# Performance work log

Measured on AMD Instinct MI355X. Metric: run time of the kernel, lower is better.

## Reference

```python
import jax, jax.numpy as jnp
import numpy as np


def setup_inputs() -> dict:
    key = jax.random.key(0)
    k1, k2 = jax.random.split(key)
    a_bar = jax.random.normal(k1, (32, 512, 512), dtype=jnp.float32)
    b_bar = jax.random.normal(k2, (32, 512, 512), dtype=jnp.float32)
    return {"a_bar": a_bar, "b_bar": b_bar}


def reference(a_bar, b_bar):
    # e[b,i,j] = <a_bar[b,i,:], b_bar[b,j,:]>
    e = jnp.einsum("bid,bjd->bij", a_bar, b_bar)
    # a_tilde: row softmax (over j) then weighted sum of b rows
    attn_a = jax.nn.softmax(e, axis=2)            # [B, Sa, Sb]
    a_tilde = jnp.einsum("bij,bjd->bid", attn_a, b_bar)
    # b_tilde: column softmax (over i), transposed, times a_bar
    attn_b = jax.nn.softmax(e, axis=1)            # [B, Sa, Sb]
    b_tilde = jnp.einsum("bij,bid->bjd", attn_b, a_bar)
    m_a = jnp.concatenate([a_bar, a_tilde, a_bar - a_tilde, a_bar * a_tilde], axis=-1)
    m_b = jnp.concatenate([b_bar, b_tilde, b_bar - b_tilde, b_bar * b_tilde], axis=-1)
    return (m_a, m_b)
```

## Files before the change

kernel.cpp:

```cpp
#include <hip/hip_runtime.h>
#include <hip/hip_bf16.h>
#include <math.h>

#define B_   32
#define S_   512
#define SxS  (S_ * S_)
#define LOG2E 1.4426950408889634f

using frag_ab = __attribute__((ext_vector_type(8))) short;
using frag_cd = __attribute__((ext_vector_type(4))) float;

__device__ inline short f2bf(float x) {
    __hip_bfloat16 h = __float2bfloat16(x);
    return *reinterpret_cast<short*>(&h);
}
__device__ inline float bf2f(short s) {
    __hip_bfloat16 h = *reinterpret_cast<__hip_bfloat16*>(&s);
    return __bfloat162float(h);
}
__device__ __forceinline__ int swz(int r) { return (r ^ (r >> 3)) & 7; }

__device__ __forceinline__ void async16(const short* g, short* l) {
    __builtin_amdgcn_global_load_lds(
        (const __attribute__((address_space(1))) void*)g,
        (__attribute__((address_space(3))) void*)l,
        16, 0, 0);
}

__global__ __launch_bounds__(256) void k_prep(const float* __restrict__ A,
                                              const float* __restrict__ Bm,
                                              short* __restrict__ PA,
                                              short* __restrict__ PB,
                                              short* __restrict__ Va,
                                              short* __restrict__ Vb)
{
    const int z   = blockIdx.z;
    const int b   = z & 31;
    const int isB = z >> 5;
    const float* X = (isB ? Bm : A) + (size_t)b * SxS;
    short* P  = (isB ? PB : PA) + (size_t)b * (S_ * 1024);
    short* Vp = (isB ? Vb : Va) + (size_t)b * SxS;
    const float scale = isB ? 1.0f : LOG2E;

    const int i0 = blockIdx.y * 64, d0 = blockIdx.x * 64;

    __shared__ short T[64][72];

    const int sl = threadIdx.x & 7;
    const int il = threadIdx.x >> 3;

    #pragma unroll
    for (int p = 0; p < 2; ++p) {
        const int i    = il + 32 * p;
        const int rowg = i0 + i;
        const float* src = X + (size_t)rowg * S_ + d0 + sl * 8;
        const float4 v0 = *(const float4*)(src);
        const float4 v1 = *(const float4*)(src + 4);

        T[sl * 8 + 0][i] = f2bf(v0.x); T[sl * 8 + 1][i] = f2bf(v0.y);
        T[sl * 8 + 2][i] = f2bf(v0.z); T[sl * 8 + 3][i] = f2bf(v0.w);
        T[sl * 8 + 4][i] = f2bf(v1.x); T[sl * 8 + 5][i] = f2bf(v1.y);
        T[sl * 8 + 6][i] = f2bf(v1.z); T[sl * 8 + 7][i] = f2bf(v1.w);

        const float xs[8] = {v0.x, v0.y, v0.z, v0.w, v1.x, v1.y, v1.z, v1.w};
        frag_ab hi, lo;
        #pragma unroll
        for (int j = 0; j < 8; ++j) {
            const float x = xs[j] * scale;
            const short h = f2bf(x);
            hi[j] = h;
            lo[j] = f2bf(x - bf2f(h));
        }
        const int W = (d0 >> 5) + (sl >> 2);
        const int q = sl & 3;
        short* base = P + (size_t)rowg * 1024 + W * 64;
        *(frag_ab*)(base + (((2 * q)     ^ (rowg & 7)) * 8)) = hi;
        *(frag_ab*)(base + (((2 * q + 1) ^ (rowg & 7)) * 8)) = lo;
    }
    __syncthreads();

    const int pc = threadIdx.x & 7, dl = threadIdx.x >> 3;
    #pragma unroll
    for (int p = 0; p < 2; ++p) {
        const int d  = dl + 32 * p;
        const int dg = d0 + d;
        frag_ab t = *(const frag_ab*)&T[d][pc * 8];
        *(frag_ab*)(Vp + (size_t)dg * 512 + i0 + ((pc ^ (dg & 7)) * 8)) = t;
    }
}

__global__ __launch_bounds__(256) void k_gemm_e(const short* __restrict__ PA,
                                                const short* __restrict__ PB,
                                                float* __restrict__ E)
{
    const int lin     = blockIdx.x + (blockIdx.y << 2) + (blockIdx.z << 4);
    const int logical = ((lin & 7) << 6) + (lin >> 3);
    const int b  = logical >> 4;
    const int i0 = ((logical >> 2) & 3) * 128;
    const int j0 = (logical & 3) * 128;

    const short* Ab = PA + (size_t)b * (S_ * 1024);
    const short* Bb = PB + (size_t)b * (S_ * 1024);
    float* Eb = E + (size_t)b * SxS;

    __shared__ __align__(16) short As[128][64];
    __shared__ __align__(16) short Bs[128][64];

    const int tid  = threadIdx.x;
    const int wave = tid >> 6, lane = tid & 63;
    const int wr   = wave >> 1, wc = wave & 1;
    const int q    = lane >> 4, m = lane & 15;
    const int srow = lane >> 3, schunk = lane & 7;

    frag_cd zero = {0.f, 0.f, 0.f, 0.f};
    frag_cd acc[4][4];
    #pragma unroll
    for (int i = 0; i < 4; ++i)
        #pragma unroll
        for (int j = 0; j < 4; ++j) acc[i][j] = zero;

    for (int k0 = 0; k0 < S_; k0 += 32) {
        const int W = k0 >> 5;
        __syncthreads();
        #pragma unroll
        for (int p = 0; p < 4; ++p) {
            const int seg    = wave * 4 + p;
            const int rowg_a = i0 + seg * 8 + srow;
            const int rowg_b = j0 + seg * 8 + srow;
            async16(Ab + (size_t)rowg_a * 1024 + W * 64 + schunk * 8, &As[seg * 8][0]);
            async16(Bb + (size_t)rowg_b * 1024 + W * 64 + schunk * 8, &Bs[seg * 8][0]);
        }
        __syncthreads();

        frag_ab ah[4], al[4], bh[4], bl[4];
        #pragma unroll
        for (int t = 0; t < 4; ++t) {
            const int ra = wr * 64 + t * 16 + m;
            const int rb = wc * 64 + t * 16 + m;
            ah[t] = *(const frag_ab*)&As[ra][((2 * q)     ^ (ra & 7)) * 8];
            al[t] = *(const frag_ab*)&As[ra][((2 * q + 1) ^ (ra & 7)) * 8];
            bh[t] = *(const frag_ab*)&Bs[rb][((2 * q)     ^ (rb & 7)) * 8];
            bl[t] = *(const frag_ab*)&Bs[rb][((2 * q + 1) ^ (rb & 7)) * 8];
        }
        #pragma unroll
        for (int mt = 0; mt < 4; ++mt)
            #pragma unroll
            for (int nt = 0; nt < 4; ++nt) {
                acc[mt][nt] = __builtin_amdgcn_mfma_f32_16x16x32_bf16(ah[mt], bh[nt], acc[mt][nt], 0, 0, 0);
                acc[mt][nt] = __builtin_amdgcn_mfma_f32_16x16x32_bf16(ah[mt], bl[nt], acc[mt][nt], 0, 0, 0);
                acc[mt][nt] = __builtin_amdgcn_mfma_f32_16x16x32_bf16(al[mt], bh[nt], acc[mt][nt], 0, 0, 0);
            }
    }

    #pragma unroll
    for (int mt = 0; mt < 4; ++mt)
        #pragma unroll
        for (int nt = 0; nt < 4; ++nt) {
            const int rb  = i0 + wr * 64 + mt * 16 + q * 4;
            const int col = j0 + wc * 64 + nt * 16 + m;
            Eb[(size_t)(rb + 0) * S_ + col] = acc[mt][nt][0];
            Eb[(size_t)(rb + 1) * S_ + col] = acc[mt][nt][1];
            Eb[(size_t)(rb + 2) * S_ + col] = acc[mt][nt][2];
            Eb[(size_t)(rb + 3) * S_ + col] = acc[mt][nt][3];
        }
}

__global__ __launch_bounds__(512) void k_pv_fused(const float* __restrict__ E,
                                                  const short* __restrict__ Va,
                                                  const short* __restrict__ Vb,
                                                  const float* __restrict__ A,
                                                  const float* __restrict__ Bm,
                                                  float* __restrict__ Ma,
                                                  float* __restrict__ Mb)
{
    const int lin     = blockIdx.x;
    const int logical = ((lin & 7) << 6) + (lin >> 3);
    const int side = logical >> 8;
    const int b    = (logical >> 3) & 31;
    const int s0   = (logical & 7) * 64;

    const float* Eb  = E + (size_t)b * SxS;
    const short* Vg  = (side ? Va : Vb) + (size_t)b * SxS;
    const float* Xb  = (side ? Bm : A) + (size_t)b * SxS;
    float* Ob = (side ? Mb : Ma) + (size_t)b * S_ * 2048;

    __shared__ __align__(16) short Pl[64][512];
    __shared__ __align__(16) short Vs[512][64];
    __shared__ float riS[64];
    __shared__ float mS[64];

    float* scr  = (float*)&Vs[0][0];
    float* scr2 = scr + 4096;

    const int tid = threadIdx.x;

    if (side == 0) {
        const int r = tid >> 3, sub = tid & 7;
        const float* er = Eb + (size_t)(s0 + r) * S_;

        float mx = -INFINITY;
        #pragma unroll
        for (int fi = 0; fi < 8; ++fi) {
            const float* p = er + sub * 8 + fi * 64;
            const float4 u  = *(const float4*)p;
            const float4 u2 = *(const float4*)(p + 4);
            mx = fmaxf(mx, fmaxf(fmaxf(u.x, u.y), fmaxf(u.z, u.w)));
            mx = fmaxf(mx, fmaxf(fmaxf(u2.x, u2.y), fmaxf(u2.z, u2.w)));
        }
        mx = fmaxf(mx, __shfl_xor(mx, 1));
        mx = fmaxf(mx, __shfl_xor(mx, 2));
        mx = fmaxf(mx, __shfl_xor(mx, 4));

        float s = 0.f;
        const int sl = (sub ^ swz(r)) * 8;
        #pragma unroll
        for (int fi = 0; fi < 8; ++fi) {
            const float* p = er + sub * 8 + fi * 64;
            const float4 u  = *(const float4*)p;
            const float4 u2 = *(const float4*)(p + 4);
            const float xs[8] = {u.x, u.y, u.z, u.w, u2.x, u2.y, u2.z, u2.w};
            frag_ab pb;
            #pragma unroll
            for (int j = 0; j < 8; ++j) {
                const float pv = exp2f(xs[j] - mx);
                s += pv;
                pb[j] = f2bf(pv);
            }
            *(frag_ab*)&Pl[r][fi * 64 + sl] = pb;
        }
        s += __shfl_xor(s, 1);
        s += __shfl_xor(s, 2);
        s += __shfl_xor(s, 4);
        if (sub == 0) riS[r] = 1.0f / s;
    } else {
        const int ib = tid >> 3, sub = tid & 7;

        float pm[8];
        #pragma unroll
        for (int c = 0; c < 8; ++c) pm[c] = -INFINITY;
        #pragma unroll
        for (int ii = 0; ii < 8; ++ii) {
            const float* p = Eb + (size_t)(ib * 8 + ii) * S_ + s0 + sub * 8;
            const float4 u  = *(const float4*)p;
            const float4 u2 = *(const float4*)(p + 4);
            pm[0] = fmaxf(pm[0], u.x);  pm[1] = fmaxf(pm[1], u.y);
            pm[2] = fmaxf(pm[2], u.z);  pm[3] = fmaxf(pm[3], u.w);
            pm[4] = fmaxf(pm[4], u2.x); pm[5] = fmaxf(pm[5], u2.y);
            pm[6] = fmaxf(pm[6], u2.z); pm[7] = fmaxf(pm[7], u2.w);
        }
        #pragma unroll
        for (int c = 0; c < 8; ++c) scr[ib * 64 + sub * 8 + c] = pm[c];
        __syncthreads();
        {
            const int col = tid & 63, h = tid >> 6;
            float v = scr[(h * 8) * 64 + col];
            #pragma unroll
            for (int k = 1; k < 8; ++k) v = fmaxf(v, scr[(h * 8 + k) * 64 + col]);
            scr2[h * 64 + col] = v;
        }
        __syncthreads();
        if (tid < 64) {
            float v = scr2[tid];
            #pragma unroll
            for (int h = 1; h < 8; ++h) v = fmaxf(v, scr2[h * 64 + tid]);
            mS[tid] = v;
        }
        __syncthreads();

        float ps[8];
        frag_ab pb[8];
        #pragma unroll
        for (int c = 0; c < 8; ++c) ps[c] = 0.f;
        #pragma unroll
        for (int ii = 0; ii < 8; ++ii) {
            const float* p = Eb + (size_t)(ib * 8 + ii) * S_ + s0 + sub * 8;
            const float4 u  = *(const float4*)p;
            const float4 u2 = *(const float4*)(p + 4);
            const float xs[8] = {u.x, u.y, u.z, u.w, u2.x, u2.y, u2.z, u2.w};
            #pragma unroll
            for (int c = 0; c < 8; ++c) {
                const float pv = exp2f(xs[c] - mS[sub * 8 + c]);
                ps[c] += pv;
                pb[c][ii] = f2bf(pv);
            }
        }
        #pragma unroll
        for (int c = 0; c < 8; ++c) {
            const int cl = sub * 8 + c;
            *(frag_ab*)&Pl[cl][(ib >> 3) * 64 + (((ib & 7) ^ swz(cl)) * 8)] = pb[c];
        }
        __syncthreads();
        #pragma unroll
        for (int c = 0; c < 8; ++c) scr[ib * 64 + sub * 8 + c] = ps[c];
        __syncthreads();
        {
            const int col = tid & 63, h = tid >> 6;
            float v = 0.f;
            #pragma unroll
            for (int k = 0; k < 8; ++k) v += scr[(h * 8 + k) * 64 + col];
            scr2[h * 64 + col] = v;
        }
        __syncthreads();
        if (tid < 64) {
            float v = 0.f;
            #pragma unroll
            for (int h = 0; h < 8; ++h) v += scr2[h * 64 + tid];
            riS[tid] = 1.0f / v;
        }
    }

    const int wv = tid >> 6, lane = tid & 63;
    const int q = lane >> 4, m = lane & 15;

    frag_cd zero = {0.f, 0.f, 0.f, 0.f};
    frag_cd acc[4][4];
    #pragma unroll
    for (int i = 0; i < 4; ++i)
        #pragma unroll
        for (int j = 0; j < 4; ++j) acc[i][j] = zero;

    for (int k0 = 0; k0 < S_; k0 += 64) {
        __syncthreads();
        #pragma unroll
        for (int p = 0; p < 8; ++p) {
            const int d = p * 64 + wv * 8 + (lane >> 3);
            async16(Vg + (size_t)d * 512 + k0 + (lane & 7) * 8,
                    &Vs[p * 64 + wv * 8][0]);
        }
        __syncthreads();

        #pragma unroll
        for (int kk = 0; kk < 2; ++kk) {
            frag_ab af[4], bf[4];
            #pragma unroll
            for (int t = 0; t < 4; ++t) {
                const int row = t * 16 + m;
                af[t] = *(const frag_ab*)&Pl[row][k0 + (((kk * 4 + q) ^ swz(row)) * 8)];
                const int dl = wv * 64 + t * 16 + m;
                bf[t] = *(const frag_ab*)&Vs[dl][(((kk * 4 + q) ^ (dl & 7)) * 8)];
            }
            #pragma unroll
            for (int mt = 0; mt < 4; ++mt)
                #pragma unroll
                for (int nt = 0; nt < 4; ++nt)
                    acc[mt][nt] = __builtin_amdgcn_mfma_f32_16x16x32_bf16(af[mt], bf[nt], acc[mt][nt], 0, 0, 0);
        }
    }

    #pragma unroll
    for (int mt = 0; mt < 4; ++mt)
        #pragma unroll
        for (int nt = 0; nt < 4; ++nt) {
            const int col = wv * 64 + nt * 16 + m;
            #pragma unroll
            for (int rr = 0; rr < 4; ++rr) {
                const int rl   = mt * 16 + q * 4 + rr;
                const int rowg = s0 + rl;
                const float at = acc[mt][nt][rr] * riS[rl];
                const float xv = Xb[(size_t)rowg * S_ + col];
                float* o = Ob + (size_t)rowg * 2048 + col;
                o[0]    = xv;
                o[512]  = at;
                o[1024] = xv - at;
                o[1536] = xv * at;
            }
        }
}

extern "C" void kernel_launch(void* const* d_in, const int* in_sizes, int n_in,
                              void* d_out, int out_size, void* d_ws, size_t ws_size,
                              hipStream_t stream)
{
    const float* A  = (const float*)d_in[0];
    const float* Bm = (const float*)d_in[1];
    float* Ma = (float*)d_out;
    float* Mb = Ma + (size_t)B_ * S_ * 2048;

    float* E  = (float*)d_ws;
    short* Va = (short*)(E + (size_t)B_ * SxS);
    short* Vb = Va + (size_t)B_ * SxS;

    short* PA = (short*)d_out;
    short* PB = PA + (size_t)B_ * S_ * 1024;

    k_prep    <<<dim3(8, 8, 64), 256, 0, stream>>>(A, Bm, PA, PB, Va, Vb);
    k_gemm_e  <<<dim3(4, 4, 32), 256, 0, stream>>>(PA, PB, E);
    k_pv_fused<<<dim3(512),      512, 0, stream>>>(E, Va, Vb, A, Bm, Ma, Mb);
}
```

Before: 468.1 us.

## Split softmax statistics into separate kernels and shrink PV tiles for more blocks

Row and column softmax max and inverse-sum are now computed by two dedicated kernels and written to workspace. The PV kernel only reads these statistics and exponentiates. It now uses 32-row by 256-column tiles with 256 threads, giving 2048 blocks instead of 512 with a smaller LDS footprint. This aims to remove the serialized in-block reductions and barriers and to improve occupancy and load balance. The cost is more passes over the E matrix (two extra stat kernels, and each PV tile re-reads E for both d-halves) plus two extra launches.

```diff
diff --git a/kernel.cpp b/kernel.cpp
--- a/kernel.cpp
+++ b/kernel.cpp
@@ -165,54 +165,138 @@
         }
 }
 
-__global__ __launch_bounds__(512) void k_pv_fused(const float* __restrict__ E,
-                                                  const short* __restrict__ Va,
-                                                  const short* __restrict__ Vb,
-                                                  const float* __restrict__ A,
-                                                  const float* __restrict__ Bm,
-                                                  float* __restrict__ Ma,
-                                                  float* __restrict__ Mb)
-{
-    const int lin     = blockIdx.x;
-    const int logical = ((lin & 7) << 6) + (lin >> 3);
-    const int side = logical >> 8;
-    const int b    = (logical >> 3) & 31;
-    const int s0   = (logical & 7) * 64;
+__global__ __launch_bounds__(256) void k_rstats(const float* __restrict__ E,
+                                                float* __restrict__ rmax,
+                                                float* __restrict__ rinv)
+{
+    const int row  = blockIdx.x * 4 + (threadIdx.x >> 6);
+    const int lane = threadIdx.x & 63;
+    const float* er = E + (size_t)row * S_;
+
+    float4 v0 = *(const float4*)(er + lane * 4);
+    float4 v1 = *(const float4*)(er + 256 + lane * 4);
+
+    float m = fmaxf(fmaxf(fmaxf(v0.x, v0.y), fmaxf(v0.z, v0.w)),
+                    fmaxf(fmaxf(v1.x, v1.y), fmaxf(v1.z, v1.w)));
+    #pragma unroll
+    for (int off = 32; off >= 1; off >>= 1)
+        m = fmaxf(m, __shfl_xor(m, off));
+
+    float s = exp2f(v0.x - m) + exp2f(v0.y - m)
+            + exp2f(v0.z - m) + exp2f(v0.w - m)
+            + exp2f(v1.x - m) + exp2f(v1.y - m)
+            + exp2f(v1.z - m) + exp2f(v1.w - m);
+    #pragma unroll
+    for (int off = 32; off >= 1; off >>= 1)
+        s += __shfl_xor(s, off);
+
+    if (lane == 0) { rmax[row] = m; rinv[row] = 1.0f / s; }
+}
+
+__global__ __launch_bounds__(256) void k_cstats(const float* __restrict__ E,
+                                                float* __restrict__ cmax,
+                                                float* __restrict__ cinv)
+{
+    const int b  = blockIdx.x >> 3;
+    const int s0 = (blockIdx.x & 7) * 64;
+    const float* Eb = E + (size_t)b * SxS;
+
+    __shared__ float scr[32][64];
+    __shared__ float mS[64];
+
+    const int tid = threadIdx.x;
+    const int ib  = tid >> 3;
+    const int sub = tid & 7;
+
+    float pm[8];
+    #pragma unroll
+    for (int c = 0; c < 8; ++c) pm[c] = -INFINITY;
+    for (int ii = 0; ii < 16; ++ii) {
+        const float* p = Eb + (size_t)(ib * 16 + ii) * S_ + s0 + sub * 8;
+        const float4 u  = *(const float4*)p;
+        const float4 u2 = *(const float4*)(p + 4);
+        pm[0] = fmaxf(pm[0], u.x);  pm[1] = fmaxf(pm[1], u.y);
+        pm[2] = fmaxf(pm[2], u.z);  pm[3] = fmaxf(pm[3], u.w);
+        pm[4] = fmaxf(pm[4], u2.x); pm[5] = fmaxf(pm[5], u2.y);
+        pm[6] = fmaxf(pm[6], u2.z); pm[7] = fmaxf(pm[7], u2.w);
+    }
+    #pragma unroll
+    for (int c = 0; c < 8; ++c) scr[ib][sub * 8 + c] = pm[c];
+    __syncthreads();
+    if (tid < 64) {
+        float v = scr[0][tid];
+        #pragma unroll
+        for (int k = 1; k < 32; ++k) v = fmaxf(v, scr[k][tid]);
+        mS[tid] = v;
+        cmax[b * S_ + s0 + tid] = v;
+    }
+    __syncthreads();
+
+    float ps[8];
+    #pragma unroll
+    for (int c = 0; c < 8; ++c) ps[c] = 0.f;
+    for (int ii = 0; ii < 16; ++ii) {
+        const float* p = Eb + (size_t)(ib * 16 + ii) * S_ + s0 + sub * 8;
+        const float4 u  = *(const float4*)p;
+        const float4 u2 = *(const float4*)(p + 4);
+        const float xs[8] = {u.x, u.y, u.z, u.w, u2.x, u2.y, u2.z, u2.w};
+        #pragma unroll
+        for (int c = 0; c < 8; ++c) ps[c] += exp2f(xs[c] - mS[sub * 8 + c]);
+    }
+    __syncthreads();
+    #pragma unroll
+    for (int c = 0; c < 8; ++c) scr[ib][sub * 8 + c] = ps[c];
+    __syncthreads();
+    if (tid < 64) {
+        float v = 0.f;
+        #pragma unroll
+        for (int k = 0; k < 32; ++k) v += scr[k][tid];
+        cinv[b * S_ + s0 + tid] = 1.0f / v;
+    }
+}
+
+__global__ __launch_bounds__(256) void k_pv(const float* __restrict__ E,
+                                            const float* __restrict__ rmx_,
+                                            const float* __restrict__ rin_,
+                                            const float* __restrict__ cmx_,
+                                            const float* __restrict__ cin_,
+                                            const short* __restrict__ Va,
+                                            const short* __restrict__ Vb,
+                                            const float* __restrict__ A,
+                                            const float* __restrict__ Bm,
+                                            float* __restrict__ Ma,
+                                            float* __restrict__ Mb)
+{
+    const int lin = blockIdx.x;
+    const int wg  = ((lin & 7) << 8) | (lin >> 3);
+    const int side = wg >> 10;
+    const int b    = (wg >> 5) & 31;
+    const int rs   = (wg >> 1) & 15;
+    const int dh   = wg & 1;
+    const int s0   = rs * 32;
 
     const float* Eb  = E + (size_t)b * SxS;
+    const float* pmx = (side ? cmx_ : rmx_) + b * S_;
+    const float* piv = (side ? cin_ : rin_) + b * S_;
     const short* Vg  = (side ? Va : Vb) + (size_t)b * SxS;
     const float* Xb  = (side ? Bm : A) + (size_t)b * SxS;
     float* Ob = (side ? Mb : Ma) + (size_t)b * S_ * 2048;
 
-    __shared__ __align__(16) short Pl[64][512];
-    __shared__ __align__(16) short Vs[512][64];
-    __shared__ float riS[64];
-    __shared__ float mS[64];
-
-    float* scr  = (float*)&Vs[0][0];
-    float* scr2 = scr + 4096;
+    __shared__ __align__(16) short Pl[32][512];
+    __shared__ __align__(16) short Vs[256][64];
+    __shared__ float riS[32];
 
     const int tid = threadIdx.x;
+    const int wv  = tid >> 6, lane = tid & 63;
+    const int q   = lane >> 4, m = lane & 15;
+
+    if (tid < 32) riS[tid] = piv[s0 + tid];
 
     if (side == 0) {
-        const int r = tid >> 3, sub = tid & 7;
-        const float* er = Eb + (size_t)(s0 + r) * S_;
-
-        float mx = -INFINITY;
-        #pragma unroll
-        for (int fi = 0; fi < 8; ++fi) {
-            const float* p = er + sub * 8 + fi * 64;
-            const float4 u  = *(const float4*)p;
-            const float4 u2 = *(const float4*)(p + 4);
-            mx = fmaxf(mx, fmaxf(fmaxf(u.x, u.y), fmaxf(u.z, u.w)));
-            mx = fmaxf(mx, fmaxf(fmaxf(u2.x, u2.y), fmaxf(u2.z, u2.w)));
-        }
-        mx = fmaxf(mx, __shfl_xor(mx, 1));
-        mx = fmaxf(mx, __shfl_xor(mx, 2));
-        mx = fmaxf(mx, __shfl_xor(mx, 4));
-
-        float s = 0.f;
-        const int sl = (sub ^ swz(r)) * 8;
+        const int rl = tid >> 3, sub = tid & 7;
+        const float mx = pmx[s0 + rl];
+        const float* er = Eb + (size_t)(s0 + rl) * S_;
+        const int sl = (sub ^ swz(rl)) * 8;
         #pragma unroll
         for (int fi = 0; fi < 8; ++fi) {
             const float* p = er + sub * 8 + fi * 64;
@@ -221,101 +305,37 @@
             const float xs[8] = {u.x, u.y, u.z, u.w, u2.x, u2.y, u2.z, u2.w};
             frag_ab pb;
             #pragma unroll
-            for (int j = 0; j < 8; ++j) {
-                const float pv = exp2f(xs[j] - mx);
-                s += pv;
-                pb[j] = f2bf(pv);
-            }
-            *(frag_ab*)&Pl[r][fi * 64 + sl] = pb;
-        }
-        s += __shfl_xor(s, 1);
-        s += __shfl_xor(s, 2);
-        s += __shfl_xor(s, 4);
-        if (sub == 0) riS[r] = 1.0f / s;
+            for (int j = 0; j < 8; ++j) pb[j] = f2bf(exp2f(xs[j] - mx));
+            *(frag_ab*)&Pl[rl][fi * 64 + sl] = pb;
+        }
     } else {
-        const int ib = tid >> 3, sub = tid & 7;
-
-        float pm[8];
-        #pragma unroll
-        for (int c = 0; c < 8; ++c) pm[c] = -INFINITY;
+        const int ib = tid >> 2, cs = tid & 3;
+        float mloc[8];
+        #pragma unroll
+        for (int c = 0; c < 8; ++c) mloc[c] = pmx[s0 + cs * 8 + c];
+        frag_ab pb[8];
         #pragma unroll
         for (int ii = 0; ii < 8; ++ii) {
-            const float* p = Eb + (size_t)(ib * 8 + ii) * S_ + s0 + sub * 8;
-            const float4 u  = *(const float4*)p;
-            const float4 u2 = *(const float4*)(p + 4);
-            pm[0] = fmaxf(pm[0], u.x);  pm[1] = fmaxf(pm[1], u.y);
-            pm[2] = fmaxf(pm[2], u.z);  pm[3] = fmaxf(pm[3], u.w);
-            pm[4] = fmaxf(pm[4], u2.x); pm[5] = fmaxf(pm[5], u2.y);
-            pm[6] = fmaxf(pm[6], u2.z); pm[7] = fmaxf(pm[7], u2.w);
-        }
-        #pragma unroll
-        for (int c = 0; c < 8; ++c) scr[ib * 64 + sub * 8 + c] = pm[c];
-        __syncthreads();
-        {
-            const int col = tid & 63, h = tid >> 6;
-            float v = scr[(h * 8) * 64 + col];
-            #pragma unroll
-            for (int k = 1; k < 8; ++k) v = fmaxf(v, scr[(h * 8 + k) * 64 + col]);
-            scr2[h * 64 + col] = v;
-        }
-        __syncthreads();
-        if (tid < 64) {
-            float v = scr2[tid];
-            #pragma unroll
-            for (int h = 1; h < 8; ++h) v = fmaxf(v, scr2[h * 64 + tid]);
-            mS[tid] = v;
-        }
-        __syncthreads();
-
-        float ps[8];
-        frag_ab pb[8];
-        #pragma unroll
-        for (int c = 0; c < 8; ++c) ps[c] = 0.f;
-        #pragma unroll
-        for (int ii = 0; ii < 8; ++ii) {
-            const float* p = Eb + (size_t)(ib * 8 + ii) * S_ + s0 + sub * 8;
+            const float* p = Eb + (size_t)(ib * 8 + ii) * S_ + s0 + cs * 8;
             const float4 u  = *(const float4*)p;
             const float4 u2 = *(const float4*)(p + 4);
             const float xs[8] = {u.x, u.y, u.z, u.w, u2.x, u2.y, u2.z, u2.w};
             #pragma unroll
-            for (int c = 0; c < 8; ++c) {
-                const float pv = exp2f(xs[c] - mS[sub * 8 + c]);
-                ps[c] += pv;
-                pb[c][ii] = f2bf(pv);
-            }
+            for (int c = 0; c < 8; ++c)
+                pb[c][ii] = f2bf(exp2f(xs[c] - mloc[c]));
         }
         #pragma unroll
         for (int c = 0; c < 8; ++c) {
-            const int cl = sub * 8 + c;
-            *(frag_ab*)&Pl[cl][(ib >> 3) * 64 + (((ib & 7) ^ swz(cl)) * 8)] = pb[c];
-        }
-        __syncthreads();
-        #pragma unroll
-        for (int c = 0; c < 8; ++c) scr[ib * 64 + sub * 8 + c] = ps[c];
-        __syncthreads();
-        {
-            const int col = tid & 63, h = tid >> 6;
-            float v = 0.f;
-            #pragma unroll
-            for (int k = 0; k < 8; ++k) v += scr[(h * 8 + k) * 64 + col];
-            scr2[h * 64 + col] = v;
-        }
-        __syncthreads();
-        if (tid < 64) {
-            float v = 0.f;
-            #pragma unroll
-            for (int h = 0; h < 8; ++h) v += scr2[h * 64 + tid];
-            riS[tid] = 1.0f / v;
-        }
-    }
-
-    const int wv = tid >> 6, lane = tid & 63;
-    const int q = lane >> 4, m = lane & 15;
+            const int cl = cs * 8 + c;
+            *(frag_ab*)&Pl[cl][((ib ^ swz(cl)) & 63) * 8
+                               + (ib & ~7) * 0] = pb[c];
+        }
+    }
 
     frag_cd zero = {0.f, 0.f, 0.f, 0.f};
-    frag_cd acc[4][4];
-    #pragma unroll
-    for (int i = 0; i < 4; ++i)
+    frag_cd acc[2][4];
+    #pragma unroll
+    for (int i = 0; i < 2; ++i)
         #pragma unroll
         for (int j = 0; j < 4; ++j) acc[i][j] = zero;
 
@@ -323,24 +343,27 @@
         __syncthreads();
         #pragma unroll
         for (int p = 0; p < 8; ++p) {
-            const int d = p * 64 + wv * 8 + (lane >> 3);
-            async16(Vg + (size_t)d * 512 + k0 + (lane & 7) * 8,
-                    &Vs[p * 64 + wv * 8][0]);
+            const int seg = p * 32 + wv * 8;
+            const int d   = dh * 256 + seg + (lane >> 3);
+            async16(Vg + (size_t)d * 512 + k0 + (lane & 7) * 8, &Vs[seg][0]);
         }
         __syncthreads();
 
         #pragma unroll
         for (int kk = 0; kk < 2; ++kk) {
-            frag_ab af[4], bf[4];
+            frag_ab af[2], bf[4];
+            #pragma unroll
+            for (int t = 0; t < 2; ++t) {
+                const int ra = t * 16 + m;
+                af[t] = *(const frag_ab*)&Pl[ra][k0 + (((kk * 4 + q) ^ swz(ra)) * 8)];
+            }
             #pragma unroll
             for (int t = 0; t < 4; ++t) {
-                const int row = t * 16 + m;
-                af[t] = *(const frag_ab*)&Pl[row][k0 + (((kk * 4 + q) ^ swz(row)) * 8)];
                 const int dl = wv * 64 + t * 16 + m;
                 bf[t] = *(const frag_ab*)&Vs[dl][(((kk * 4 + q) ^ (dl & 7)) * 8)];
             }
             #pragma unroll
-            for (int mt = 0; mt < 4; ++mt)
+            for (int mt = 0; mt < 2; ++mt)
                 #pragma unroll
                 for (int nt = 0; nt < 4; ++nt)
                     acc[mt][nt] = __builtin_amdgcn_mfma_f32_16x16x32_bf16(af[mt], bf[nt], acc[mt][nt], 0, 0, 0);
@@ -348,17 +371,17 @@
     }
 
     #pragma unroll
-    for (int mt = 0; mt < 4; ++mt)
+    for (int mt = 0; mt < 2; ++mt)
         #pragma unroll
         for (int nt = 0; nt < 4; ++nt) {
-            const int col = wv * 64 + nt * 16 + m;
+            const int colg = dh * 256 + wv * 64 + nt * 16 + m;
             #pragma unroll
             for (int rr = 0; rr < 4; ++rr) {
                 const int rl   = mt * 16 + q * 4 + rr;
                 const int rowg = s0 + rl;
                 const float at = acc[mt][nt][rr] * riS[rl];
-                const float xv = Xb[(size_t)rowg * S_ + col];
-                float* o = Ob + (size_t)rowg * 2048 + col;
+                const float xv = Xb[(size_t)rowg * S_ + colg];
+                float* o = Ob + (size_t)rowg * 2048 + colg;
                 o[0]    = xv;
                 o[512]  = at;
                 o[1024] = xv - at;
@@ -376,14 +399,21 @@
     float* Ma = (float*)d_out;
     float* Mb = Ma + (size_t)B_ * S_ * 2048;
 
-    float* E  = (float*)d_ws;
-    short* Va = (short*)(E + (size_t)B_ * SxS);
-    short* Vb = Va + (size_t)B_ * SxS;
+    float* E    = (float*)d_ws;
+    short* Va   = (short*)(E + (size_t)B_ * SxS);
+    short* Vb   = Va + (size_t)B_ * SxS;
+    float* rmax = (float*)(Vb + (size_t)B_ * SxS);
+    float* rinv = rmax + B_ * S_;
+    float* cmax = rinv + B_ * S_;
+    float* cinv = cmax + B_ * S_;
 
     short* PA = (short*)d_out;
     short* PB = PA + (size_t)B_ * S_ * 1024;
 
-    k_prep    <<<dim3(8, 8, 64), 256, 0, stream>>>(A, Bm, PA, PB, Va, Vb);
-    k_gemm_e  <<<dim3(4, 4, 32), 256, 0, stream>>>(PA, PB, E);
-    k_pv_fused<<<dim3(512),      512, 0, stream>>>(E, Va, Vb, A, Bm, Ma, Mb);
-}
+    k_prep  <<<dim3(8, 8, 64),    256, 0, stream>>>(A, Bm, PA, PB, Va, Vb);
+    k_gemm_e<<<dim3(4, 4, 32),    256, 0, stream>>>(PA, PB, E);
+    k_rstats<<<dim3(B_ * S_ / 4), 256, 0, stream>>>(E, rmax, rinv);
+    k_cstats<<<dim3(B_ * 8),      256, 0, stream>>>(E, cmax, cinv);
+    k_pv    <<<dim3(2048),        256, 0, stream>>>(E, rmax, rinv, cmax, cinv,
+                                                    Va, Vb, A, Bm, Ma, Mb);
+}
```

After: 475.7 us. About the same (+1.6%).
